# Performance work log

Measured on AMD Instinct MI355X. Metric: run time of the kernel, lower is better.

Reference implementation:

```python
import jax, jax.numpy as jnp
import numpy as np

B, N, F, H = 64, 1024, 128, 256  # graphs, nodes per graph, nfeat, nhid


def setup_inputs() -> dict:
    key = jax.random.key(0)
    ks = jax.random.split(key, 8)
    s_in = 1.0 / np.sqrt(F)
    s_h = 1.0 / np.sqrt(H)
    return {
        "embs": jax.random.normal(ks[0], (B, N, F), jnp.float32),
        "adjmat": jax.random.uniform(ks[1], (B, N, N), jnp.float32) / N,  # row-scaled dense adjacency
        "W0": jax.random.normal(ks[2], (F, H), jnp.float32) * s_in,
        "b0": jnp.zeros((H,), jnp.float32),
        "W1": jax.random.normal(ks[3], (H, H), jnp.float32) * s_h,
        "b1": jnp.zeros((H,), jnp.float32),
        "W2": jax.random.normal(ks[4], (H, H), jnp.float32) * s_h,
        "b2": jnp.zeros((H,), jnp.float32),
        "Wl": jax.random.normal(ks[5], (H, F), jnp.float32) * s_h,
        "bl": jnp.zeros((F,), jnp.float32),
    }


def reference(embs, adjmat, W0, b0, W1, b1, W2, b2, Wl, bl):
    # Batched form of the per-graph loop: every adj is N x N, so the
    # x[:adj.shape[0]] slice is identity and all graphs fuse into one GEMM.
    hid = embs  # [B, N, F]
    for W, b in ((W0, b0), (W1, b1), (W2, b2)):
        # GraphConvolution: adj @ (x @ W) + b, then relu
        hid = jax.nn.relu(jnp.einsum('bnm,bmh->bnh', adjmat, hid @ W) + b)
    out = hid @ Wl + bl          # [B, N, F] linear_hid
    return out[:, 0, :]          # hid[0] per graph -> [B, F]
```

## Files before the change

kernel.cpp:

```cpp
#include <hip/hip_runtime.h>
#include <stdint.h>

typedef __bf16 bf16;
typedef __bf16 bf16x8 __attribute__((ext_vector_type(8)));
typedef float f32x4 __attribute__((ext_vector_type(4)));

enum { EPI_STORE = 0, EPI_BIAS_RELU = 1, EPI_VRED = 2 };

template<bool A_F32, bool B_F32, int EPI>
__global__ __launch_bounds__(256, 2)
void gemm_bt(const void* __restrict__ Ap, const void* __restrict__ Btp,
             const float* __restrict__ bias, bf16* __restrict__ C,
             float* __restrict__ vpart, const float* __restrict__ adjp,
             int K, int ldA, int ldBt, int ldC,
             long sA, long sBt, long sC)
{
  constexpr int BM = 128, BN = 256, BK = 32;
  __shared__ __align__(16) bf16 As[BM * BK];
  __shared__ __align__(16) bf16 Bs[BN * BK];
  __shared__ float a0s[BM];
  __shared__ float vsum[BN];

  const int tid  = threadIdx.x;
  const int lane = tid & 63;
  const int wid  = tid >> 6;
  const int wm   = wid >> 1;
  const int wn   = wid & 1;
  const int l15  = lane & 15;
  const int quad = lane >> 4;

  const int nb = blockIdx.x, mb = blockIdx.y, g = blockIdx.z;

  const long aoff = (long)g * sA + (long)mb * BM * ldA;
  const long boff = (long)g * sBt + (long)nb * BN * ldBt;

  if constexpr (EPI == EPI_VRED) {
    if (tid < BM) a0s[tid] = adjp[(long)g * sA + mb * BM + tid];
    vsum[tid] = 0.f;
  }

  f32x4 acc[4][8] = {};

  const int nsteps = K / BK;
  const int r  = tid >> 2;
  const int kc = (tid & 3) * 8;

  for (int ks = 0; ks < nsteps; ++ks) {
    const int k0 = ks * BK;
    __syncthreads();
    if constexpr (A_F32) {
      const float* Ag = (const float*)Ap + aoff + k0;
      #pragma unroll
      for (int p = 0; p < BM / 64; ++p) {
        const float4* s = (const float4*)(Ag + (long)(p * 64 + r) * ldA + kc);
        float4 v0 = s[0], v1 = s[1];
        bf16x8 w;
        w[0]=(bf16)v0.x; w[1]=(bf16)v0.y; w[2]=(bf16)v0.z; w[3]=(bf16)v0.w;
        w[4]=(bf16)v1.x; w[5]=(bf16)v1.y; w[6]=(bf16)v1.z; w[7]=(bf16)v1.w;
        *(bf16x8*)&As[p * 2048 + tid * 8] = w;
      }
    } else {
      const bf16* Ag = (const bf16*)Ap + aoff + k0;
      #pragma unroll
      for (int p = 0; p < BM / 64; ++p)
        *(bf16x8*)&As[p * 2048 + tid * 8] =
            *(const bf16x8*)(Ag + (long)(p * 64 + r) * ldA + kc);
    }
    if constexpr (B_F32) {
      const float* Bg = (const float*)Btp + boff + k0;
      #pragma unroll
      for (int p = 0; p < BN / 64; ++p) {
        const float4* s = (const float4*)(Bg + (long)(p * 64 + r) * ldBt + kc);
        float4 v0 = s[0], v1 = s[1];
        bf16x8 w;
        w[0]=(bf16)v0.x; w[1]=(bf16)v0.y; w[2]=(bf16)v0.z; w[3]=(bf16)v0.w;
        w[4]=(bf16)v1.x; w[5]=(bf16)v1.y; w[6]=(bf16)v1.z; w[7]=(bf16)v1.w;
        *(bf16x8*)&Bs[p * 2048 + tid * 8] = w;
      }
    } else {
      const bf16* Bg = (const bf16*)Btp + boff + k0;
      #pragma unroll
      for (int p = 0; p < BN / 64; ++p)
        *(bf16x8*)&Bs[p * 2048 + tid * 8] =
            *(const bf16x8*)(Bg + (long)(p * 64 + r) * ldBt + kc);
    }
    __syncthreads();

    bf16x8 af[4], bfr[8];
    #pragma unroll
    for (int i = 0; i < 4; ++i)
      af[i] = *(const bf16x8*)&As[(wm * 64 + i * 16 + l15) * BK + quad * 8];
    #pragma unroll
    for (int j = 0; j < 8; ++j)
      bfr[j] = *(const bf16x8*)&Bs[(wn * 128 + j * 16 + l15) * BK + quad * 8];
    #pragma unroll
    for (int i = 0; i < 4; ++i)
      #pragma unroll
      for (int j = 0; j < 8; ++j)
        acc[i][j] = __builtin_amdgcn_mfma_f32_16x16x32_bf16(af[i], bfr[j], acc[i][j], 0, 0, 0);
  }

  if constexpr (EPI == EPI_STORE || EPI == EPI_BIAS_RELU) {
    bf16* Cg = C + (long)g * sC;
    #pragma unroll
    for (int i = 0; i < 4; ++i) {
      const int row0 = mb * BM + wm * 64 + i * 16 + quad * 4;
      #pragma unroll
      for (int j = 0; j < 8; ++j) {
        const int col = nb * BN + wn * 128 + j * 16 + l15;
        float bv = 0.f;
        if constexpr (EPI == EPI_BIAS_RELU) bv = bias[col];
        #pragma unroll
        for (int rr = 0; rr < 4; ++rr) {
          float v = acc[i][j][rr];
          if constexpr (EPI == EPI_BIAS_RELU) v = fmaxf(v + bv, 0.f);
          Cg[(long)(row0 + rr) * ldC + col] = (bf16)v;
        }
      }
    }
  } else {
    __syncthreads();
    #pragma unroll
    for (int j = 0; j < 8; ++j) {
      const int col = wn * 128 + j * 16 + l15;
      const float bv = bias[col];
      float p = 0.f;
      #pragma unroll
      for (int i = 0; i < 4; ++i) {
        const int lr = wm * 64 + i * 16 + quad * 4;
        #pragma unroll
        for (int rr = 0; rr < 4; ++rr)
          p += fmaxf(acc[i][j][rr] + bv, 0.f) * a0s[lr + rr];
      }
      atomicAdd(&vsum[col], p);
    }
    __syncthreads();
    vpart[((long)g * 8 + mb) * 256 + tid] = vsum[tid];
  }
}

__global__ void prep_w(const float* __restrict__ W0, const float* __restrict__ W1,
                       bf16* __restrict__ W0t, bf16* __restrict__ W1t)
{
  const int idx = blockIdx.x * 256 + threadIdx.x;
  if (idx < 256 * 128) {
    const int h = idx >> 7, k = idx & 127;
    W0t[idx] = (bf16)W0[k * 256 + h];
  }
  const int h = idx >> 8, k = idx & 255;
  W1t[idx] = (bf16)W1[k * 256 + h];
}

__global__ void finish_k(const float* __restrict__ vpart, const float* __restrict__ W2,
                         const float* __restrict__ b2, const float* __restrict__ Wl,
                         const float* __restrict__ bl, float* __restrict__ out)
{
  const int b = blockIdx.x, t = threadIdx.x;
  __shared__ float v[256], h3[256];
  float s = 0.f;
  #pragma unroll
  for (int mb = 0; mb < 8; ++mb) s += vpart[((long)b * 8 + mb) * 256 + t];
  v[t] = s;
  __syncthreads();
  float z = b2[t];
  for (int k = 0; k < 256; ++k) z += v[k] * W2[k * 256 + t];
  h3[t] = fmaxf(z, 0.f);
  __syncthreads();
  if (t < 128) {
    float o = bl[t];
    for (int h = 0; h < 256; ++h) o += h3[h] * Wl[h * 128 + t];
    out[(long)b * 128 + t] = o;
  }
}

extern "C" void kernel_launch(void* const* d_in, const int* in_sizes, int n_in,
                              void* d_out, int out_size, void* d_ws, size_t ws_size,
                              hipStream_t stream) {
  const float* embs = (const float*)d_in[0];
  const float* adj  = (const float*)d_in[1];
  const float* W0   = (const float*)d_in[2];
  const float* b0   = (const float*)d_in[3];
  const float* W1   = (const float*)d_in[4];
  const float* b1   = (const float*)d_in[5];
  const float* W2   = (const float*)d_in[6];
  const float* b2   = (const float*)d_in[7];
  const float* Wl   = (const float*)d_in[8];
  const float* bl   = (const float*)d_in[9];
  float* out = (float*)d_out;

  char* ws = (char*)d_ws;
  bf16*  Zt    = (bf16*)(ws);
  bf16*  Hb    = (bf16*)(ws + 33554432);
  bf16*  W0t   = (bf16*)(ws + 67108864);
  bf16*  W1t   = (bf16*)(ws + 67174400);
  float* vpart = (float*)(ws + 67305472);

  prep_w<<<256, 256, 0, stream>>>(W0, W1, W0t, W1t);

  gemm_bt<false, true, EPI_STORE><<<dim3(4, 2, 64), 256, 0, stream>>>(
      W0t, embs, nullptr, Zt, nullptr, nullptr,
      128, 128, 128, 1024, 0L, 131072L, 262144L);

  gemm_bt<true, false, EPI_BIAS_RELU><<<dim3(1, 8, 64), 256, 0, stream>>>(
      adj, Zt, b0, Hb, nullptr, nullptr,
      1024, 1024, 1024, 256, 1048576L, 262144L, 262144L);

  gemm_bt<false, false, EPI_STORE><<<dim3(4, 2, 64), 256, 0, stream>>>(
      W1t, Hb, nullptr, Zt, nullptr, nullptr,
      256, 256, 256, 1024, 0L, 262144L, 262144L);

  gemm_bt<true, false, EPI_VRED><<<dim3(1, 8, 64), 256, 0, stream>>>(
      adj, Zt, b1, nullptr, vpart, adj,
      1024, 1024, 1024, 256, 1048576L, 262144L, 0L);

  finish_k<<<64, 256, 0, stream>>>(vpart, W2, b2, Wl, bl, out);
}
```

Before: 568.2 us.

## Double-buffer GEMM tiles, use direct global-to-LDS loads, cache bf16 adjacency for reuse

The GEMM main loop now double-buffers the shared-memory tiles. Global loads for the next K step are issued before the current step's MFMAs, and conversion and storing happen afterwards, so memory latency overlaps compute. bf16 operands load straight into LDS via global_load_lds. The first adjacency GEMM also writes a bf16 copy of adj to workspace, which the second adjacency GEMM reads instead of the fp32 original, halving its traffic. The catch is twice the LDS per block, more registers for prefetch, extra write traffic, and a dependence on a large workspace being available.

```diff
diff --git a/kernel.cpp b/kernel.cpp
--- a/kernel.cpp
+++ b/kernel.cpp
@@ -7,17 +7,24 @@
 
 enum { EPI_STORE = 0, EPI_BIAS_RELU = 1, EPI_VRED = 2 };
 
-template<bool A_F32, bool B_F32, int EPI>
+__device__ __forceinline__ void gload16(const bf16* g, bf16* l) {
+  __builtin_amdgcn_global_load_lds(
+      (const __attribute__((address_space(1))) unsigned int*)g,
+      (__attribute__((address_space(3))) unsigned int*)l, 16, 0, 0);
+}
+
+template<bool A_F32, bool B_F32, int EPI, bool WRITE_A16>
 __global__ __launch_bounds__(256, 2)
 void gemm_bt(const void* __restrict__ Ap, const void* __restrict__ Btp,
              const float* __restrict__ bias, bf16* __restrict__ C,
              float* __restrict__ vpart, const float* __restrict__ adjp,
+             bf16* __restrict__ A16,
              int K, int ldA, int ldBt, int ldC,
              long sA, long sBt, long sC)
 {
   constexpr int BM = 128, BN = 256, BK = 32;
-  __shared__ __align__(16) bf16 As[BM * BK];
-  __shared__ __align__(16) bf16 Bs[BN * BK];
+  __shared__ __align__(16) bf16 As[2][BM * BK];
+  __shared__ __align__(16) bf16 Bs[2][BN * BK];
   __shared__ float a0s[BM];
   __shared__ float vsum[BN];
 
@@ -39,65 +46,97 @@
     vsum[tid] = 0.f;
   }
 
-  f32x4 acc[4][8] = {};
-
-  const int nsteps = K / BK;
   const int r  = tid >> 2;
   const int kc = (tid & 3) * 8;
 
-  for (int ks = 0; ks < nsteps; ++ks) {
+  float4 pfA[4];
+  float4 pfB[8];
+
+  auto issue = [&](int ks, int buf) {
     const int k0 = ks * BK;
-    __syncthreads();
     if constexpr (A_F32) {
       const float* Ag = (const float*)Ap + aoff + k0;
       #pragma unroll
       for (int p = 0; p < BM / 64; ++p) {
         const float4* s = (const float4*)(Ag + (long)(p * 64 + r) * ldA + kc);
-        float4 v0 = s[0], v1 = s[1];
+        pfA[p * 2 + 0] = s[0];
+        pfA[p * 2 + 1] = s[1];
+      }
+    } else {
+      const bf16* Ag = (const bf16*)Ap + aoff + k0;
+      #pragma unroll
+      for (int p = 0; p < BM / 64; ++p)
+        gload16(Ag + (long)(p * 64 + r) * ldA + kc, &As[buf][p * 2048 + tid * 8]);
+    }
+    if constexpr (B_F32) {
+      const float* Bg = (const float*)Btp + boff + k0;
+      #pragma unroll
+      for (int p = 0; p < BN / 64; ++p) {
+        const float4* s = (const float4*)(Bg + (long)(p * 64 + r) * ldBt + kc);
+        pfB[p * 2 + 0] = s[0];
+        pfB[p * 2 + 1] = s[1];
+      }
+    } else {
+      const bf16* Bg = (const bf16*)Btp + boff + k0;
+      #pragma unroll
+      for (int p = 0; p < BN / 64; ++p)
+        gload16(Bg + (long)(p * 64 + r) * ldBt + kc, &Bs[buf][p * 2048 + tid * 8]);
+    }
+  };
+
+  auto commit = [&](int ks, int buf) {
+    if constexpr (A_F32) {
+      #pragma unroll
+      for (int p = 0; p < BM / 64; ++p) {
+        float4 v0 = pfA[p * 2 + 0], v1 = pfA[p * 2 + 1];
         bf16x8 w;
         w[0]=(bf16)v0.x; w[1]=(bf16)v0.y; w[2]=(bf16)v0.z; w[3]=(bf16)v0.w;
         w[4]=(bf16)v1.x; w[5]=(bf16)v1.y; w[6]=(bf16)v1.z; w[7]=(bf16)v1.w;
-        *(bf16x8*)&As[p * 2048 + tid * 8] = w;
-      }
-    } else {
-      const bf16* Ag = (const bf16*)Ap + aoff + k0;
-      #pragma unroll
-      for (int p = 0; p < BM / 64; ++p)
-        *(bf16x8*)&As[p * 2048 + tid * 8] =
-            *(const bf16x8*)(Ag + (long)(p * 64 + r) * ldA + kc);
+        *(bf16x8*)&As[buf][p * 2048 + tid * 8] = w;
+        if constexpr (WRITE_A16)
+          *(bf16x8*)&A16[aoff + (long)(p * 64 + r) * ldA + ks * BK + kc] = w;
+      }
     }
     if constexpr (B_F32) {
-      const float* Bg = (const float*)Btp + boff + k0;
       #pragma unroll
       for (int p = 0; p < BN / 64; ++p) {
-        const float4* s = (const float4*)(Bg + (long)(p * 64 + r) * ldBt + kc);
-        float4 v0 = s[0], v1 = s[1];
+        float4 v0 = pfB[p * 2 + 0], v1 = pfB[p * 2 + 1];
         bf16x8 w;
         w[0]=(bf16)v0.x; w[1]=(bf16)v0.y; w[2]=(bf16)v0.z; w[3]=(bf16)v0.w;
         w[4]=(bf16)v1.x; w[5]=(bf16)v1.y; w[6]=(bf16)v1.z; w[7]=(bf16)v1.w;
-        *(bf16x8*)&Bs[p * 2048 + tid * 8] = w;
-      }
-    } else {
-      const bf16* Bg = (const bf16*)Btp + boff + k0;
-      #pragma unroll
-      for (int p = 0; p < BN / 64; ++p)
-        *(bf16x8*)&Bs[p * 2048 + tid * 8] =
-            *(const bf16x8*)(Bg + (long)(p * 64 + r) * ldBt + kc);
-    }
-    __syncthreads();
+        *(bf16x8*)&Bs[buf][p * 2048 + tid * 8] = w;
+      }
+    }
+  };
+
+  f32x4 acc[4][8] = {};
+  const int nsteps = K / BK;
+
+  issue(0, 0);
+  commit(0, 0);
+  __syncthreads();
+
+  int cur = 0;
+  for (int ks = 0; ks < nsteps; ++ks) {
+    const bool pf = (ks + 1 < nsteps);
+    if (pf) issue(ks + 1, cur ^ 1);
 
     bf16x8 af[4], bfr[8];
     #pragma unroll
     for (int i = 0; i < 4; ++i)
-      af[i] = *(const bf16x8*)&As[(wm * 64 + i * 16 + l15) * BK + quad * 8];
+      af[i] = *(const bf16x8*)&As[cur][(wm * 64 + i * 16 + l15) * BK + quad * 8];
     #pragma unroll
     for (int j = 0; j < 8; ++j)
-      bfr[j] = *(const bf16x8*)&Bs[(wn * 128 + j * 16 + l15) * BK + quad * 8];
+      bfr[j] = *(const bf16x8*)&Bs[cur][(wn * 128 + j * 16 + l15) * BK + quad * 8];
     #pragma unroll
     for (int i = 0; i < 4; ++i)
       #pragma unroll
       for (int j = 0; j < 8; ++j)
         acc[i][j] = __builtin_amdgcn_mfma_f32_16x16x32_bf16(af[i], bfr[j], acc[i][j], 0, 0, 0);
+
+    if (pf) commit(ks + 1, cur ^ 1);
+    __syncthreads();
+    cur ^= 1;
   }
 
   if constexpr (EPI == EPI_STORE || EPI == EPI_BIAS_RELU) {
@@ -194,24 +233,38 @@
   bf16*  W0t   = (bf16*)(ws + 67108864);
   bf16*  W1t   = (bf16*)(ws + 67174400);
   float* vpart = (float*)(ws + 67305472);
+  bf16*  adj16 = (bf16*)(ws + 134217728);
+  const bool useA16 = ws_size >= (size_t)268435456;
 
   prep_w<<<256, 256, 0, stream>>>(W0, W1, W0t, W1t);
 
-  gemm_bt<false, true, EPI_STORE><<<dim3(4, 2, 64), 256, 0, stream>>>(
-      W0t, embs, nullptr, Zt, nullptr, nullptr,
+  gemm_bt<false, true, EPI_STORE, false><<<dim3(4, 2, 64), 256, 0, stream>>>(
+      W0t, embs, nullptr, Zt, nullptr, nullptr, nullptr,
       128, 128, 128, 1024, 0L, 131072L, 262144L);
 
-  gemm_bt<true, false, EPI_BIAS_RELU><<<dim3(1, 8, 64), 256, 0, stream>>>(
-      adj, Zt, b0, Hb, nullptr, nullptr,
-      1024, 1024, 1024, 256, 1048576L, 262144L, 262144L);
-
-  gemm_bt<false, false, EPI_STORE><<<dim3(4, 2, 64), 256, 0, stream>>>(
-      W1t, Hb, nullptr, Zt, nullptr, nullptr,
+  if (useA16) {
+    gemm_bt<true, false, EPI_BIAS_RELU, true><<<dim3(1, 8, 64), 256, 0, stream>>>(
+        adj, Zt, b0, Hb, nullptr, nullptr, adj16,
+        1024, 1024, 1024, 256, 1048576L, 262144L, 262144L);
+  } else {
+    gemm_bt<true, false, EPI_BIAS_RELU, false><<<dim3(1, 8, 64), 256, 0, stream>>>(
+        adj, Zt, b0, Hb, nullptr, nullptr, nullptr,
+        1024, 1024, 1024, 256, 1048576L, 262144L, 262144L);
+  }
+
+  gemm_bt<false, false, EPI_STORE, false><<<dim3(4, 2, 64), 256, 0, stream>>>(
+      W1t, Hb, nullptr, Zt, nullptr, nullptr, nullptr,
       256, 256, 256, 1024, 0L, 262144L, 262144L);
 
-  gemm_bt<true, false, EPI_VRED><<<dim3(1, 8, 64), 256, 0, stream>>>(
-      adj, Zt, b1, nullptr, vpart, adj,
-      1024, 1024, 1024, 256, 1048576L, 262144L, 0L);
+  if (useA16) {
+    gemm_bt<false, false, EPI_VRED, false><<<dim3(1, 8, 64), 256, 0, stream>>>(
+        adj16, Zt, b1, nullptr, vpart, adj, nullptr,
+        1024, 1024, 1024, 256, 1048576L, 262144L, 0L);
+  } else {
+    gemm_bt<true, false, EPI_VRED, false><<<dim3(1, 8, 64), 256, 0, stream>>>(
+        adj, Zt, b1, nullptr, vpart, adj, nullptr,
+        1024, 1024, 1024, 256, 1048576L, 262144L, 0L);
+  }
 
   finish_k<<<64, 256, 0, stream>>>(vpart, W2, b2, Wl, bl, out);
 }
```

After: 592.2 us. +4.2%, slower.

## Pre-convert inputs to bf16 and double-buffer GEMM tiles via direct global-to-LDS loads

Applied to the files above, without the earlier changes.

Adds a conversion kernel that turns the fp32 adjacency and embeddings into bf16 once, so every GEMM reads bf16 operands. The GEMM main loop now uses global_load_lds into two LDS buffers, prefetching the next K-step while the current one computes. A XOR swizzle on the K-chunk is applied to cut LDS bank conflicts. The cost is an extra full pass over the 256MB adjacency to write a 128MB bf16 copy, and the pipeline relies on hand-written vmcnt and barrier sequences.

```diff
diff --git a/kernel.cpp b/kernel.cpp
--- a/kernel.cpp
+++ b/kernel.cpp
@@ -7,17 +7,24 @@
 
 enum { EPI_STORE = 0, EPI_BIAS_RELU = 1, EPI_VRED = 2 };
 
-template<bool A_F32, bool B_F32, int EPI>
+__device__ __forceinline__ void gload16(const bf16* g, bf16* l) {
+  __builtin_amdgcn_global_load_lds(
+      (const __attribute__((address_space(1))) unsigned int*)g,
+      (__attribute__((address_space(3))) unsigned int*)l, 16, 0, 0);
+}
+
+template<int EPI>
 __global__ __launch_bounds__(256, 2)
-void gemm_bt(const void* __restrict__ Ap, const void* __restrict__ Btp,
+void gemm_bt(const bf16* __restrict__ Ap, const bf16* __restrict__ Btp,
              const float* __restrict__ bias, bf16* __restrict__ C,
              float* __restrict__ vpart, const float* __restrict__ adjp,
              int K, int ldA, int ldBt, int ldC,
              long sA, long sBt, long sC)
 {
   constexpr int BM = 128, BN = 256, BK = 32;
-  __shared__ __align__(16) bf16 As[BM * BK];
-  __shared__ __align__(16) bf16 Bs[BN * BK];
+  static_assert(BM / 64 + BN / 64 == 6, "vmcnt(6) assumes 6 gloads/thread/step");
+  __shared__ __align__(16) bf16 As[2][BM * BK];
+  __shared__ __align__(16) bf16 Bs[2][BN * BK];
   __shared__ float a0s[BM];
   __shared__ float vsum[BN];
 
@@ -39,65 +46,54 @@
     vsum[tid] = 0.f;
   }
 
+  const int r   = tid >> 2;
+  const int kcs = (((tid & 3) ^ ((tid >> 3) & 3)) << 3);
+
+  const bf16* Ag0 = Ap + aoff;
+  const bf16* Bg0 = Btp + boff;
+
+  auto issueG = [&](int s, int buf) {
+    const int k0 = s * BK;
+    #pragma unroll
+    for (int p = 0; p < BM / 64; ++p)
+      gload16(Ag0 + (long)(p * 64 + r) * ldA + k0 + kcs, &As[buf][p * 2048 + tid * 8]);
+    #pragma unroll
+    for (int p = 0; p < BN / 64; ++p)
+      gload16(Bg0 + (long)(p * 64 + r) * ldBt + k0 + kcs, &Bs[buf][p * 2048 + tid * 8]);
+  };
+
+  const int csw = ((quad ^ ((l15 >> 1) & 3)) << 3);
+
   f32x4 acc[4][8] = {};
-
   const int nsteps = K / BK;
-  const int r  = tid >> 2;
-  const int kc = (tid & 3) * 8;
-
-  for (int ks = 0; ks < nsteps; ++ks) {
-    const int k0 = ks * BK;
-    __syncthreads();
-    if constexpr (A_F32) {
-      const float* Ag = (const float*)Ap + aoff + k0;
-      #pragma unroll
-      for (int p = 0; p < BM / 64; ++p) {
-        const float4* s = (const float4*)(Ag + (long)(p * 64 + r) * ldA + kc);
-        float4 v0 = s[0], v1 = s[1];
-        bf16x8 w;
-        w[0]=(bf16)v0.x; w[1]=(bf16)v0.y; w[2]=(bf16)v0.z; w[3]=(bf16)v0.w;
-        w[4]=(bf16)v1.x; w[5]=(bf16)v1.y; w[6]=(bf16)v1.z; w[7]=(bf16)v1.w;
-        *(bf16x8*)&As[p * 2048 + tid * 8] = w;
-      }
+
+  issueG(0, 0);
+  int cur = 0;
+  for (int s = 0; s < nsteps; ++s) {
+    if (s + 1 < nsteps) {
+      issueG(s + 1, cur ^ 1);
+      asm volatile("s_waitcnt vmcnt(6)" ::: "memory");
     } else {
-      const bf16* Ag = (const bf16*)Ap + aoff + k0;
-      #pragma unroll
-      for (int p = 0; p < BM / 64; ++p)
-        *(bf16x8*)&As[p * 2048 + tid * 8] =
-            *(const bf16x8*)(Ag + (long)(p * 64 + r) * ldA + kc);
+      asm volatile("s_waitcnt vmcnt(0)" ::: "memory");
     }
-    if constexpr (B_F32) {
-      const float* Bg = (const float*)Btp + boff + k0;
-      #pragma unroll
-      for (int p = 0; p < BN / 64; ++p) {
-        const float4* s = (const float4*)(Bg + (long)(p * 64 + r) * ldBt + kc);
-        float4 v0 = s[0], v1 = s[1];
-        bf16x8 w;
-        w[0]=(bf16)v0.x; w[1]=(bf16)v0.y; w[2]=(bf16)v0.z; w[3]=(bf16)v0.w;
-        w[4]=(bf16)v1.x; w[5]=(bf16)v1.y; w[6]=(bf16)v1.z; w[7]=(bf16)v1.w;
-        *(bf16x8*)&Bs[p * 2048 + tid * 8] = w;
-      }
-    } else {
-      const bf16* Bg = (const bf16*)Btp + boff + k0;
-      #pragma unroll
-      for (int p = 0; p < BN / 64; ++p)
-        *(bf16x8*)&Bs[p * 2048 + tid * 8] =
-            *(const bf16x8*)(Bg + (long)(p * 64 + r) * ldBt + kc);
-    }
-    __syncthreads();
+    __builtin_amdgcn_s_barrier();
 
     bf16x8 af[4], bfr[8];
     #pragma unroll
     for (int i = 0; i < 4; ++i)
-      af[i] = *(const bf16x8*)&As[(wm * 64 + i * 16 + l15) * BK + quad * 8];
+      af[i] = *(const bf16x8*)&As[cur][(wm * 64 + i * 16 + l15) * BK + csw];
     #pragma unroll
     for (int j = 0; j < 8; ++j)
-      bfr[j] = *(const bf16x8*)&Bs[(wn * 128 + j * 16 + l15) * BK + quad * 8];
+      bfr[j] = *(const bf16x8*)&Bs[cur][(wn * 128 + j * 16 + l15) * BK + csw];
+    asm volatile("s_waitcnt lgkmcnt(0)" ::: "memory");
+    __builtin_amdgcn_s_barrier();
+
     #pragma unroll
     for (int i = 0; i < 4; ++i)
       #pragma unroll
       for (int j = 0; j < 8; ++j)
         acc[i][j] = __builtin_amdgcn_mfma_f32_16x16x32_bf16(af[i], bfr[j], acc[i][j], 0, 0, 0);
+    cur ^= 1;
   }
 
   if constexpr (EPI == EPI_STORE || EPI == EPI_BIAS_RELU) {
@@ -139,6 +135,22 @@
   }
 }
 
+__global__ void cvt2(const float* __restrict__ a, bf16* __restrict__ ao, long na8,
+                     const float* __restrict__ b, bf16* __restrict__ bo, long nb8)
+{
+  const long stride = (long)gridDim.x * blockDim.x;
+  for (long i = (long)blockIdx.x * blockDim.x + threadIdx.x; i < na8 + nb8; i += stride) {
+    const float* src; bf16* dst; long k;
+    if (i < na8) { src = a; dst = ao; k = i; } else { src = b; dst = bo; k = i - na8; }
+    const float4* s = (const float4*)(src + k * 8);
+    float4 v0 = s[0], v1 = s[1];
+    bf16x8 w;
+    w[0]=(bf16)v0.x; w[1]=(bf16)v0.y; w[2]=(bf16)v0.z; w[3]=(bf16)v0.w;
+    w[4]=(bf16)v1.x; w[5]=(bf16)v1.y; w[6]=(bf16)v1.z; w[7]=(bf16)v1.w;
+    *(bf16x8*)(dst + k * 8) = w;
+  }
+}
+
 __global__ void prep_w(const float* __restrict__ W0, const float* __restrict__ W1,
                        bf16* __restrict__ W0t, bf16* __restrict__ W1t)
 {
@@ -189,28 +201,33 @@
   float* out = (float*)d_out;
 
   char* ws = (char*)d_ws;
-  bf16*  Zt    = (bf16*)(ws);
-  bf16*  Hb    = (bf16*)(ws + 33554432);
-  bf16*  W0t   = (bf16*)(ws + 67108864);
-  bf16*  W1t   = (bf16*)(ws + 67174400);
-  float* vpart = (float*)(ws + 67305472);
+  bf16*  Zt     = (bf16*)(ws);
+  bf16*  Hb     = (bf16*)(ws + 33554432);
+  bf16*  W0t    = (bf16*)(ws + 67108864);
+  bf16*  W1t    = (bf16*)(ws + 67174400);
+  float* vpart  = (float*)(ws + 67305472);
+  bf16*  embs16 = (bf16*)(ws + 67829760);
+  bf16*  adj16  = (bf16*)(ws + 134217728);
 
   prep_w<<<256, 256, 0, stream>>>(W0, W1, W0t, W1t);
 
-  gemm_bt<false, true, EPI_STORE><<<dim3(4, 2, 64), 256, 0, stream>>>(
-      W0t, embs, nullptr, Zt, nullptr, nullptr,
+  cvt2<<<2048, 256, 0, stream>>>(adj, adj16, 64L * 1024 * 1024 / 8,
+                                 embs, embs16, 64L * 1024 * 128 / 8);
+
+  gemm_bt<EPI_STORE><<<dim3(4, 2, 64), 256, 0, stream>>>(
+      W0t, embs16, nullptr, Zt, nullptr, nullptr,
       128, 128, 128, 1024, 0L, 131072L, 262144L);
 
-  gemm_bt<true, false, EPI_BIAS_RELU><<<dim3(1, 8, 64), 256, 0, stream>>>(
-      adj, Zt, b0, Hb, nullptr, nullptr,
+  gemm_bt<EPI_BIAS_RELU><<<dim3(1, 8, 64), 256, 0, stream>>>(
+      adj16, Zt, b0, Hb, nullptr, nullptr,
       1024, 1024, 1024, 256, 1048576L, 262144L, 262144L);
 
-  gemm_bt<false, false, EPI_STORE><<<dim3(4, 2, 64), 256, 0, stream>>>(
+  gemm_bt<EPI_STORE><<<dim3(4, 2, 64), 256, 0, stream>>>(
       W1t, Hb, nullptr, Zt, nullptr, nullptr,
       256, 256, 256, 1024, 0L, 262144L, 262144L);
 
-  gemm_bt<true, false, EPI_VRED><<<dim3(1, 8, 64), 256, 0, stream>>>(
-      adj, Zt, b1, nullptr, vpart, adj,
+  gemm_bt<EPI_VRED><<<dim3(1, 8, 64), 256, 0, stream>>>(
+      adj16, Zt, b1, nullptr, vpart, adj,
       1024, 1024, 1024, 256, 1048576L, 262144L, 0L);
 
   finish_k<<<64, 256, 0, stream>>>(vpart, W2, b2, Wl, bl, out);
```

New measurement: 616.3 us. 8.5% more time.
